# Optimization experiments

Measured on AMD Instinct MI355X. Metric: run time of the kernel, lower is better.

Reference implementation:

```python
import jax, jax.numpy as jnp
import numpy as np

# Architecture constants (from module defaults)
D, H, DH, P, G, DEPTH, M, NCLS = 192, 3, 64, 16, 14, 12, 128, 1000  # M = feature_map_dim // 2
EXITS = (4, 8, 12)
TEMP = 1.0 / np.sqrt(DH)  # Favor softmax_temp = 1/sqrt(d_head)
EPS_ATTN = 1e-6           # fast_transformers LinearAttention eps
LN_EPS = 1e-5


def ln(x, g, b):
    mu = x.mean(-1, keepdims=True)
    var = ((x - mu) ** 2).mean(-1, keepdims=True)
    return (x - mu) * jax.lax.rsqrt(var + LN_EPS) * g + b


def favor(x, omega):
    # FAVOR+ positive random features for the softmax kernel.
    # x: [B,L,H,DH], omega: [DH,M] -> phi: [B,L,H,2M]
    xs = x * np.float32(np.sqrt(TEMP))
    off = 0.5 * (xs * xs).sum(-1, keepdims=True)
    u = jnp.einsum('blhd,dm->blhm', xs, omega)
    phi = jnp.concatenate([jnp.exp(u - off), jnp.exp(-u - off)], axis=-1)
    return phi * np.float32(1.0 / np.sqrt(2 * M))


def forward(x, patch_w, patch_b, pe_ln_g, pe_ln_b, cls_token, pos_embed,
            Wq, bq, Wk, bk, Wv, bv, Wo, bo,
            ln1_g, ln1_b, ln2_g, ln2_b, lnb_g, lnb_b,
            W1, b1, W2, b2, omega, head_w, head_b):
    B = x.shape[0]
    # Patch embedding: Conv2d(k=16, s=16) == blocked einsum
    xp = x.reshape(B, 3, G, P, G, P)
    tok = jnp.einsum('bchpwq,dcpq->bhwd', xp, patch_w).reshape(B, G * G, D) + patch_b
    tok = ln(tok, pe_ln_g, pe_ln_b)  # PatchEmbed.norm (norm_layer=LayerNorm)
    tok = jnp.concatenate([jnp.broadcast_to(cls_token, (B, 1, D)), tok], axis=1) + pos_embed
    xc = tok  # [B, 197, D]
    outs = []
    for i in range(DEPTH):
        # --- linear (FAVOR) attention ---
        q = (xc @ Wq[i].T + bq[i]).reshape(B, -1, H, DH)
        k = (xc @ Wk[i].T + bk[i]).reshape(B, -1, H, DH)
        v = (xc @ Wv[i].T + bv[i]).reshape(B, -1, H, DH)
        Qp = favor(q, omega[i])
        Kp = favor(k, omega[i])
        KV = jnp.einsum('bshm,bshd->bhmd', Kp, v)
        Z = 1.0 / (jnp.einsum('blhm,bhm->blh', Qp, Kp.sum(axis=1)) + EPS_ATTN)
        attn = jnp.einsum('blhm,bhmd,blh->blhd', Qp, KV, Z).reshape(B, -1, D)
        # fast_transformers TransformerEncoderLayer (post-norm style)
        xc = xc + attn @ Wo[i].T + bo[i]
        y = xc = ln(xc, ln1_g[i], ln1_b[i])
        y = jax.nn.relu(y @ W1[i].T + b1[i]) @ W2[i].T + b2[i]
        xc = ln(xc + y, ln2_g[i], ln2_b[i])
        # per-block TransformerEncoder final norm (builder final_normalization)
        xc = ln(xc, lnb_g[i], lnb_b[i])
        if (i + 1) in EXITS:
            j = EXITS.index(i + 1)
            z = xc.mean(axis=1)  # AdaptiveAvgPool1d(1) over sequence
            outs.append(z @ head_w[j].T + head_b[j])
    return tuple(outs)


def setup_inputs() -> dict:
    key = jax.random.key(0)
    ks = iter(jax.random.split(key, 32))
    n = lambda shape, s=0.02: jax.random.normal(next(ks), shape, jnp.float32) * s
    return dict(
        x=jax.random.normal(next(ks), (64, 3, 224, 224), jnp.float32),
        patch_w=n((D, 3, P, P)), patch_b=jnp.zeros((D,), jnp.float32),
        pe_ln_g=jnp.ones((D,), jnp.float32), pe_ln_b=jnp.zeros((D,), jnp.float32),
        cls_token=n((1, 1, D)), pos_embed=n((1, G * G + 1, D)),
        Wq=n((DEPTH, D, D)), bq=jnp.zeros((DEPTH, D), jnp.float32),
        Wk=n((DEPTH, D, D)), bk=jnp.zeros((DEPTH, D), jnp.float32),
        Wv=n((DEPTH, D, D)), bv=jnp.zeros((DEPTH, D), jnp.float32),
        Wo=n((DEPTH, D, D)), bo=jnp.zeros((DEPTH, D), jnp.float32),
        ln1_g=jnp.ones((DEPTH, D), jnp.float32), ln1_b=jnp.zeros((DEPTH, D), jnp.float32),
        ln2_g=jnp.ones((DEPTH, D), jnp.float32), ln2_b=jnp.zeros((DEPTH, D), jnp.float32),
        lnb_g=jnp.ones((DEPTH, D), jnp.float32), lnb_b=jnp.zeros((DEPTH, D), jnp.float32),
        W1=n((DEPTH, 4 * D, D)), b1=jnp.zeros((DEPTH, 4 * D), jnp.float32),
        W2=n((DEPTH, D, 4 * D)), b2=jnp.zeros((DEPTH, D), jnp.float32),
        omega=jax.random.normal(next(ks), (DEPTH, DH, M), jnp.float32),
        head_w=n((len(EXITS), NCLS, D)), head_b=jnp.zeros((len(EXITS), NCLS), jnp.float32),
    )


def reference(x, patch_w, patch_b, pe_ln_g, pe_ln_b, cls_token, pos_embed,
              Wq, bq, Wk, bk, Wv, bv, Wo, bo,
              ln1_g, ln1_b, ln2_g, ln2_b, lnb_g, lnb_b,
              W1, b1, W2, b2, omega, head_w, head_b):
    return forward(x, patch_w, patch_b, pe_ln_g, pe_ln_b, cls_token, pos_embed,
                   Wq, bq, Wk, bk, Wv, bv, Wo, bo,
                   ln1_g, ln1_b, ln2_g, ln2_b, lnb_g, lnb_b,
                   W1, b1, W2, b2, omega, head_w, head_b)
```

## Files before the change

kernel.cpp:

```cpp
#include <hip/hip_runtime.h>
#include <math.h>

#define BB     64
#define LLEN   197
#define BLROWS 12608
#define MPAD   12672
#define DMODEL 192
#define NHEAD  3
#define DHEAD  64
#define M2FEAT 256
#define FFDIM  768
#define NDEPTH 12
#define NCLS   1000
#define NPATCH 196
#define BPROWS 12544
#define KPATCH 768
#define PHIRS  264

#define MODE_PLAIN 0
#define MODE_RELU  1

typedef unsigned short ushort;
typedef __attribute__((ext_vector_type(8))) short bf16x8;
typedef __attribute__((ext_vector_type(4))) float floatx4;
typedef __attribute__((ext_vector_type(4))) short short4v;

__device__ __forceinline__ float wave_reduce_sum(float v) {
#pragma unroll
  for (int s = 32; s > 0; s >>= 1) v += __shfl_xor(v, s, 64);
  return v;
}
__device__ __forceinline__ ushort f2bf(float f) {
  unsigned u = __float_as_uint(f);
  return (ushort)((u + 0x7fffu + ((u >> 16) & 1u)) >> 16);
}
__device__ __forceinline__ float bf2f(ushort u) {
  return __uint_as_float(((unsigned)u) << 16);
}
__device__ __forceinline__ void gll16(const ushort* g, ushort* l) {
  __builtin_amdgcn_global_load_lds(
      (const __attribute__((address_space(1))) void*)g,
      (__attribute__((address_space(3))) void*)l, 16, 0, 0);
}

__global__ __launch_bounds__(256) void gemm_128(
    const ushort* __restrict__ A, int lda,
    const ushort* __restrict__ W, int ldw,
    const float* __restrict__ bias,
    ushort* __restrict__ C, int ldc, int Ndim, int Kdim, int mode)
{
  __shared__ __align__(16) ushort As[2][128 * 32];
  __shared__ __align__(16) ushort Ws[2][128 * 32];
  const int tid = threadIdx.x;
  const int bm = blockIdx.x, bn = blockIdx.y;
  const int wave = tid >> 6, lane = tid & 63;
  const int wm = (wave >> 1) * 64, wn = (wave & 1) * 64;
  const int quad = lane >> 4, l16 = lane & 15;
  const int lrow = lane >> 2, lk = (lane & 3) * 8;
  const ushort* Ap = A + (size_t)(bm * 128) * lda;
  const ushort* Wp = W + (size_t)(bn * 128) * ldw;
  floatx4 acc[4][4] = {};
  const int nT = Kdim >> 5;
#pragma unroll
  for (int t = 0; t < 2; ++t) {
    const int rb = (t * 4 + wave) * 16;
    gll16(Ap + (size_t)(rb + lrow) * lda + lk, &As[0][rb * 32]);
    gll16(Wp + (size_t)(rb + lrow) * ldw + lk, &Ws[0][rb * 32]);
  }
  for (int kt = 0; kt < nT; ++kt) {
    const int cur = kt & 1;
    __syncthreads();
    if (kt + 1 < nT) {
      const int kk = (kt + 1) * 32, nxt = cur ^ 1;
#pragma unroll
      for (int t = 0; t < 2; ++t) {
        const int rb = (t * 4 + wave) * 16;
        gll16(Ap + (size_t)(rb + lrow) * lda + kk + lk, &As[nxt][rb * 32]);
        gll16(Wp + (size_t)(rb + lrow) * ldw + kk + lk, &Ws[nxt][rb * 32]);
      }
    }
    bf16x8 af[4], bf[4];
#pragma unroll
    for (int i = 0; i < 4; ++i) {
      af[i] = *(const bf16x8*)&As[cur][(wm + i * 16 + l16) * 32 + quad * 8];
      bf[i] = *(const bf16x8*)&Ws[cur][(wn + i * 16 + l16) * 32 + quad * 8];
    }
#pragma unroll
    for (int i = 0; i < 4; ++i)
#pragma unroll
      for (int j = 0; j < 4; ++j)
        acc[i][j] = __builtin_amdgcn_mfma_f32_16x16x32_bf16(af[i], bf[j], acc[i][j], 0, 0, 0);
  }
#pragma unroll
  for (int j = 0; j < 4; ++j) {
    const int col = bn * 128 + wn + j * 16 + l16;
    if (col >= Ndim) continue;
    const float bv = bias[col];
#pragma unroll
    for (int i = 0; i < 4; ++i)
#pragma unroll
      for (int r = 0; r < 4; ++r) {
        const int grow = bm * 128 + wm + i * 16 + quad * 4 + r;
        float o = acc[i][j][r] + bv;
        if (mode == MODE_RELU) o = fmaxf(o, 0.f);
        C[(size_t)grow * ldc + col] = f2bf(o);
      }
  }
}

__global__ __launch_bounds__(256) void gemm_bf2(
    const ushort* __restrict__ A, int lda,
    const ushort* __restrict__ W, int ldw,
    const float* __restrict__ bias,
    ushort* __restrict__ C, int ldc, int Kdim, int mode)
{
  __shared__ __align__(16) ushort As[2][128 * 32];
  __shared__ __align__(16) ushort Ws[2][64 * 32];
  const int tid = threadIdx.x;
  const int bm = blockIdx.x, bn = blockIdx.y;
  const int wave = tid >> 6, lane = tid & 63;
  const int wm = (wave >> 1) * 64, wn = (wave & 1) * 32;
  const int quad = lane >> 4, l16 = lane & 15;
  const int lrow = lane >> 2, lk = (lane & 3) * 8;
  const ushort* Ap = A + (size_t)(bm * 128) * lda;
  const ushort* Wp = W + (size_t)(bn * 64) * ldw;
  floatx4 acc[4][2] = {};
  const int nT = Kdim >> 5;
#pragma unroll
  for (int t = 0; t < 2; ++t) {
    const int rb = (t * 4 + wave) * 16;
    gll16(Ap + (size_t)(rb + lrow) * lda + lk, &As[0][rb * 32]);
  }
  gll16(Wp + (size_t)(wave * 16 + lrow) * ldw + lk, &Ws[0][wave * 16 * 32]);
  for (int kt = 0; kt < nT; ++kt) {
    const int cur = kt & 1;
    __syncthreads();
    if (kt + 1 < nT) {
      const int kk = (kt + 1) * 32, nxt = cur ^ 1;
#pragma unroll
      for (int t = 0; t < 2; ++t) {
        const int rb = (t * 4 + wave) * 16;
        gll16(Ap + (size_t)(rb + lrow) * lda + kk + lk, &As[nxt][rb * 32]);
      }
      gll16(Wp + (size_t)(wave * 16 + lrow) * ldw + kk + lk, &Ws[nxt][wave * 16 * 32]);
    }
    bf16x8 af[4], bf[2];
#pragma unroll
    for (int i = 0; i < 4; ++i)
      af[i] = *(const bf16x8*)&As[cur][(wm + i * 16 + l16) * 32 + quad * 8];
#pragma unroll
    for (int j = 0; j < 2; ++j)
      bf[j] = *(const bf16x8*)&Ws[cur][(wn + j * 16 + l16) * 32 + quad * 8];
#pragma unroll
    for (int i = 0; i < 4; ++i)
#pragma unroll
      for (int j = 0; j < 2; ++j)
        acc[i][j] = __builtin_amdgcn_mfma_f32_16x16x32_bf16(af[i], bf[j], acc[i][j], 0, 0, 0);
  }
#pragma unroll
  for (int j = 0; j < 2; ++j) {
    const int col = bn * 64 + wn + j * 16 + l16;
    const float bv = bias[col];
#pragma unroll
    for (int i = 0; i < 4; ++i)
#pragma unroll
      for (int r = 0; r < 4; ++r) {
        const int grow = bm * 128 + wm + i * 16 + quad * 4 + r;
        float o = acc[i][j][r] + bv;
        if (mode == MODE_RELU) o = fmaxf(o, 0.f);
        C[(size_t)grow * ldc + col] = f2bf(o);
      }
  }
}

__global__ __launch_bounds__(256) void gemm_ln(
    const ushort* __restrict__ A, int lda,
    const ushort* __restrict__ W, int ldw,
    const float* __restrict__ bias,
    ushort* __restrict__ XC,
    const float* __restrict__ ga, const float* __restrict__ ba,
    const float* __restrict__ gb, const float* __restrict__ bb,
    int Kdim, int dln)
{
  __shared__ __align__(16) ushort As[2][64 * 32];
  __shared__ __align__(16) ushort Ws[2][192 * 32];
  const int tid = threadIdx.x;
  const int bm = blockIdx.x;
  const int wave = tid >> 6, lane = tid & 63;
  const int quad = lane >> 4, l16 = lane & 15;
  const int lrow = lane >> 2, lk = (lane & 3) * 8;
  const ushort* Ap = A + (size_t)(bm * 64) * lda;
  floatx4 acc[12] = {};
  const int nT = Kdim >> 5;
  gll16(Ap + (size_t)(wave * 16 + lrow) * lda + lk, &As[0][wave * 16 * 32]);
#pragma unroll
  for (int t = 0; t < 3; ++t) {
    const int rb = wave * 48 + t * 16;
    gll16(W + (size_t)(rb + lrow) * ldw + lk, &Ws[0][rb * 32]);
  }
  for (int kt = 0; kt < nT; ++kt) {
    const int cur = kt & 1;
    __syncthreads();
    if (kt + 1 < nT) {
      const int kk = (kt + 1) * 32, nxt = cur ^ 1;
      gll16(Ap + (size_t)(wave * 16 + lrow) * lda + kk + lk, &As[nxt][wave * 16 * 32]);
#pragma unroll
      for (int t = 0; t < 3; ++t) {
        const int rb = wave * 48 + t * 16;
        gll16(W + (size_t)(rb + lrow) * ldw + kk + lk, &Ws[nxt][rb * 32]);
      }
    }
    const bf16x8 af = *(const bf16x8*)&As[cur][(wave * 16 + l16) * 32 + quad * 8];
#pragma unroll
    for (int j = 0; j < 12; ++j) {
      const bf16x8 bf = *(const bf16x8*)&Ws[cur][(j * 16 + l16) * 32 + quad * 8];
      acc[j] = __builtin_amdgcn_mfma_f32_16x16x32_bf16(af, bf, acc[j], 0, 0, 0);
    }
  }
#pragma unroll
  for (int r = 0; r < 4; ++r) {
    const int row = bm * 64 + wave * 16 + quad * 4 + r;
    ushort* xp = XC + (size_t)row * DMODEL;
    float xr[12];
    float s = 0.f, sq = 0.f;
#pragma unroll
    for (int j = 0; j < 12; ++j) {
      const int col = j * 16 + l16;
      const float o = acc[j][r] + bias[col] + bf2f(xp[col]);
      xr[j] = o; s += o; sq += o * o;
    }
#pragma unroll
    for (int m = 1; m < 16; m <<= 1) {
      s += __shfl_xor(s, m, 64); sq += __shfl_xor(sq, m, 64);
    }
    float mu = s * (1.f / 192.f);
    float var = sq * (1.f / 192.f) - mu * mu;
    float rs = rsqrtf(var + 1e-5f);
#pragma unroll
    for (int j = 0; j < 12; ++j) {
      const int col = j * 16 + l16;
      xr[j] = (xr[j] - mu) * rs * ga[col] + ba[col];
    }
    if (dln) {
      float s2 = 0.f, sq2 = 0.f;
#pragma unroll
      for (int j = 0; j < 12; ++j) { s2 += xr[j]; sq2 += xr[j] * xr[j]; }
#pragma unroll
      for (int m = 1; m < 16; m <<= 1) {
        s2 += __shfl_xor(s2, m, 64); sq2 += __shfl_xor(sq2, m, 64);
      }
      mu = s2 * (1.f / 192.f);
      var = sq2 * (1.f / 192.f) - mu * mu;
      rs = rsqrtf(var + 1e-5f);
#pragma unroll
      for (int j = 0; j < 12; ++j) {
        const int col = j * 16 + l16;
        xr[j] = (xr[j] - mu) * rs * gb[col] + bb[col];
      }
    }
#pragma unroll
    for (int j = 0; j < 12; ++j) xp[j * 16 + l16] = f2bf(xr[j]);
  }
}

__global__ __launch_bounds__(256) void kv_fused(
    const ushort* __restrict__ qkv, const ushort* __restrict__ OmT,
    ushort* __restrict__ KVt)
{
  __shared__ __align__(16) ushort Ks[32 * 64];
  __shared__ __align__(16) ushort Vs[32 * 64];
  __shared__ __align__(16) ushort Om[64 * 64];
  __shared__ __align__(16) ushort PhT[128 * 32];
  __shared__ __align__(16) ushort Vts[80 * 32];
  __shared__ float offs[32];
  const int tid = threadIdx.x;
  const int bh = blockIdx.x, mh = blockIdx.y;
  const int b = bh / 3, h = bh - b * 3;
  const int wave = tid >> 6, lane = tid & 63;
  const int quad = lane >> 4, l16 = lane & 15;
  const int lr8 = lane >> 3, lk8 = (lane & 7) * 8;
#pragma unroll
  for (int t = 0; t < 2; ++t) {
    const int rb = (t * 4 + wave) * 8;
    gll16(OmT + (size_t)(mh * 64 + rb + lr8) * 64 + lk8, &Om[rb * 64]);
  }
  {
    const int rb = wave * 8;
    const int l = rb + lr8;
    gll16(qkv + (size_t)(b * 197 + l) * 576 + 192 + h * 64 + lk8, &Ks[rb * 64]);
    gll16(qkv + (size_t)(b * 197 + l) * 576 + 384 + h * 64 + lk8, &Vs[rb * 64]);
  }
  floatx4 acc[2][5] = {};
  for (int c = 0; c < 7; ++c) {
    const int l0 = c * 32;
    __syncthreads();
    if (tid < 64) {
      const int row = tid >> 1, half = tid & 1;
      float s = 0.f;
#pragma unroll
      for (int t = 0; t < 4; ++t) {
        bf16x8 v8 = *(const bf16x8*)&Ks[row * 64 + half * 32 + t * 8];
#pragma unroll
        for (int q = 0; q < 8; ++q) { float xv = bf2f((ushort)v8[q]); s += xv * xv; }
      }
      s += __shfl_xor(s, 1, 64);
      if (half == 0) offs[row] = 0.0625f * s;
    }
    for (int e = tid; e < 80 * 32; e += 256) {
      const int d = e >> 5, ll = e & 31;
      ushort v = 0;
      if (l0 + ll < 197) {
        if (d < 64) v = Vs[ll * 64 + d];
        else if (d == 64) v = 0x3F80;
      }
      Vts[d * 32 + ll] = v;
    }
    floatx4 ui[2] = {};
#pragma unroll
    for (int ks = 0; ks < 64; ks += 32) {
      bf16x8 af[2], bfm;
#pragma unroll
      for (int i = 0; i < 2; ++i)
        af[i] = *(const bf16x8*)&Ks[(i * 16 + l16) * 64 + ks + quad * 8];
      bfm = *(const bf16x8*)&Om[(wave * 16 + l16) * 64 + ks + quad * 8];
#pragma unroll
      for (int i = 0; i < 2; ++i)
        ui[i] = __builtin_amdgcn_mfma_f32_16x16x32_bf16(af[i], bfm, ui[i], 0, 0, 0);
    }
    __syncthreads();
    {
      const int mloc = wave * 16 + l16;
#pragma unroll
      for (int i = 0; i < 2; ++i) {
#pragma unroll
        for (int r = 0; r < 4; ++r) {
          const int ll = i * 16 + quad * 4 + r;
          float ep = 0.f, em = 0.f;
          if (l0 + ll < 197) {
            const float off = offs[ll];
            const float u = ui[i][r];
            ep = __expf(u - off) * 0.0625f;
            em = __expf(-u - off) * 0.0625f;
          }
          PhT[mloc * 32 + ll] = f2bf(ep);
          PhT[(64 + mloc) * 32 + ll] = f2bf(em);
        }
      }
    }
    if (c + 1 < 7) {
      const int rb = wave * 8;
      const int l = (c + 1) * 32 + rb + lr8;
      gll16(qkv + (size_t)(b * 197 + l) * 576 + 192 + h * 64 + lk8, &Ks[rb * 64]);
      gll16(qkv + (size_t)(b * 197 + l) * 576 + 384 + h * 64 + lk8, &Vs[rb * 64]);
    }
    __syncthreads();
    bf16x8 af[2], bf[5];
#pragma unroll
    for (int i = 0; i < 2; ++i)
      af[i] = *(const bf16x8*)&PhT[(wave * 32 + i * 16 + l16) * 32 + quad * 8];
#pragma unroll
    for (int j = 0; j < 5; ++j)
      bf[j] = *(const bf16x8*)&Vts[(j * 16 + l16) * 32 + quad * 8];
#pragma unroll
    for (int i = 0; i < 2; ++i)
#pragma unroll
      for (int j = 0; j < 5; ++j)
        acc[i][j] = __builtin_amdgcn_mfma_f32_16x16x32_bf16(af[i], bf[j], acc[i][j], 0, 0, 0);
  }
#pragma unroll
  for (int i = 0; i < 2; ++i) {
    const int prow0 = wave * 32 + i * 16 + quad * 4;
    const int f0 = (prow0 < 64) ? (mh * 64 + prow0) : (128 + mh * 64 + prow0 - 64);
#pragma unroll
    for (int j = 0; j < 5; ++j) {
      const int d = j * 16 + l16;
      short4v pk;
#pragma unroll
      for (int r = 0; r < 4; ++r) pk[r] = (short)f2bf(acc[i][j][r]);
      *(short4v*)(KVt + ((size_t)bh * 80 + d) * 256 + f0) = pk;
    }
  }
}

__global__ __launch_bounds__(256) void attn_fused(
    const ushort* __restrict__ qkv, const ushort* __restrict__ OmT,
    const ushort* __restrict__ KVt, ushort* __restrict__ OUT)
{
  __shared__ __align__(16) ushort Phi[128 * PHIRS];
  __shared__ __align__(16) ushort Bs[2][80 * 32];
  __shared__ float offs[128];
  __shared__ float zs[128];
  ushort* Qs = Phi;
  ushort* Om = Phi + 128 * 64;
  const int tid = threadIdx.x;
  const int bx = blockIdx.x, bh = blockIdx.y;
  const int b = bh / 3, h = bh - b * 3;
  const int wave = tid >> 6, lane = tid & 63;
  const int wm = (wave >> 1) * 64, wn = (wave & 1) * 64;
  const int quad = lane >> 4, l16 = lane & 15;
  const int lr8 = lane >> 3, lk8 = (lane & 7) * 8;
  const int lrow = lane >> 2, lk = (lane & 3) * 8;
#pragma unroll
  for (int t = 0; t < 4; ++t) {
    const int rb = (t * 4 + wave) * 8;
    const int l = bx * 128 + rb + lr8;
    gll16(qkv + (size_t)(b * 197 + l) * 576 + h * 64 + lk8, &Qs[rb * 64]);
    gll16(OmT + (size_t)(rb + lr8) * 64 + lk8, &Om[rb * 64]);
  }
  __syncthreads();
  {
    const int row = tid >> 1, half = tid & 1;
    float s = 0.f;
#pragma unroll
    for (int t = 0; t < 4; ++t) {
      bf16x8 v8 = *(const bf16x8*)&Qs[row * 64 + half * 32 + t * 8];
#pragma unroll
      for (int q = 0; q < 8; ++q) { float xv = bf2f((ushort)v8[q]); s += xv * xv; }
    }
    s += __shfl_xor(s, 1, 64);
    if (half == 0) offs[row] = 0.0625f * s;
  }
  floatx4 uacc[4][4] = {};
#pragma unroll
  for (int ks = 0; ks < 64; ks += 32) {
    bf16x8 af[4], bf[4];
#pragma unroll
    for (int i = 0; i < 4; ++i) {
      af[i] = *(const bf16x8*)&Qs[(wm + i * 16 + l16) * 64 + ks + quad * 8];
      bf[i] = *(const bf16x8*)&Om[(wn + i * 16 + l16) * 64 + ks + quad * 8];
    }
#pragma unroll
    for (int i = 0; i < 4; ++i)
#pragma unroll
      for (int j = 0; j < 4; ++j)
        uacc[i][j] = __builtin_amdgcn_mfma_f32_16x16x32_bf16(af[i], bf[j], uacc[i][j], 0, 0, 0);
  }
  __syncthreads();
#pragma unroll
  for (int i = 0; i < 4; ++i) {
#pragma unroll
    for (int r = 0; r < 4; ++r) {
      const int l = wm + i * 16 + quad * 4 + r;
      const float off = offs[l];
#pragma unroll
      for (int j = 0; j < 4; ++j) {
        const int m = wn + j * 16 + l16;
        const float u = uacc[i][j][r];
        Phi[l * PHIRS + m]       = f2bf(__expf(u - off)  * 0.0625f);
        Phi[l * PHIRS + m + 128] = f2bf(__expf(-u - off) * 0.0625f);
      }
    }
  }
  const ushort* Bp = KVt + (size_t)bh * 80 * 256;
  gll16(Bp + (size_t)(wave * 16 + lrow) * 256 + lk, &Bs[0][wave * 16 * 32]);
  if (wave == 0) gll16(Bp + (size_t)(64 + lrow) * 256 + lk, &Bs[0][64 * 32]);
  floatx4 acc[2][5] = {};
  for (int c = 0; c < 8; ++c) {
    const int cur = c & 1;
    __syncthreads();
    if (c + 1 < 8) {
      const int m0 = (c + 1) * 32, nxt = cur ^ 1;
      gll16(Bp + (size_t)(wave * 16 + lrow) * 256 + m0 + lk, &Bs[nxt][wave * 16 * 32]);
      if (wave == 0) gll16(Bp + (size_t)(64 + lrow) * 256 + m0 + lk, &Bs[nxt][64 * 32]);
    }
    const int m0 = c * 32;
    bf16x8 af[2], bf[5];
#pragma unroll
    for (int i = 0; i < 2; ++i)
      af[i] = *(const bf16x8*)&Phi[(wave * 32 + i * 16 + l16) * PHIRS + m0 + quad * 8];
#pragma unroll
    for (int j = 0; j < 5; ++j)
      bf[j] = *(const bf16x8*)&Bs[cur][(j * 16 + l16) * 32 + quad * 8];
#pragma unroll
    for (int i = 0; i < 2; ++i)
#pragma unroll
      for (int j = 0; j < 5; ++j)
        acc[i][j] = __builtin_amdgcn_mfma_f32_16x16x32_bf16(af[i], bf[j], acc[i][j], 0, 0, 0);
  }
  if (l16 == 0) {
#pragma unroll
    for (int i = 0; i < 2; ++i)
#pragma unroll
      for (int r = 0; r < 4; ++r)
        zs[wave * 32 + i * 16 + quad * 4 + r] = acc[i][4][r];
  }
  __syncthreads();
#pragma unroll
  for (int i = 0; i < 2; ++i) {
#pragma unroll
    for (int r = 0; r < 4; ++r) {
      const int ll = wave * 32 + i * 16 + quad * 4 + r;
      const int l = bx * 128 + ll;
      if (l >= 197) continue;
      const float z = 1.f / (zs[ll] + 1e-6f);
#pragma unroll
      for (int j = 0; j < 4; ++j)
        OUT[(size_t)(b * 197 + l) * 192 + h * 64 + j * 16 + l16] =
            f2bf(acc[i][j][r] * z);
    }
  }
}

__global__ void conv_qkv(const float* __restrict__ Wq, const float* __restrict__ Wk,
                         const float* __restrict__ Wv, const float* __restrict__ bq,
                         const float* __restrict__ bk, const float* __restrict__ bv,
                         ushort* __restrict__ dst, float* __restrict__ bdst) {
  const int l = blockIdx.y;
  const int e = blockIdx.x * 256 + threadIdx.x;
  const int n = e / 192, k = e - n * 192;
  const float* src;
  if (n < 192)      src = Wq + (size_t)l * 36864 + n * 192;
  else if (n < 384) src = Wk + (size_t)l * 36864 + (n - 192) * 192;
  else              src = Wv + (size_t)l * 36864 + (n - 384) * 192;
  dst[(size_t)l * 640 * 192 + e] = f2bf(src[k]);
  if (e < 576) {
    float bvv;
    if (e < 192)      bvv = bq[l * 192 + e];
    else if (e < 384) bvv = bk[l * 192 + e - 192];
    else              bvv = bv[l * 192 + e - 384];
    bdst[l * 576 + e] = bvv;
  }
}

__global__ void conv_pad(const float* __restrict__ src, ushort* __restrict__ dst,
                         int NK, int padNK) {
  const int l = blockIdx.y;
  const int e = blockIdx.x * 256 + threadIdx.x;
  if (e < NK) dst[(size_t)l * padNK + e] = f2bf(src[(size_t)l * NK + e]);
}

__global__ void conv_omt(const float* __restrict__ om, ushort* __restrict__ dst) {
  const int l = blockIdx.y;
  const int e = blockIdx.x * 256 + threadIdx.x;
  const int m = e >> 6, d = e & 63;
  dst[(size_t)l * 8192 + e] = f2bf(0.35355339059327379f * om[(size_t)l * 8192 + d * 128 + m]);
}

__global__ __launch_bounds__(256) void im2col_kernel(
    const float* __restrict__ X, ushort* __restrict__ Apd)
{
  const int bp = blockIdx.x;
  const int b = bp / NPATCH, p = bp - b * NPATCH;
  const int gh = p / 14, gw = p - gh * 14;
  for (int e = threadIdx.x; e < KPATCH; e += 256) {
    const int c = e >> 8, rem = e & 255, ph = rem >> 4, pw = rem & 15;
    Apd[(size_t)bp * KPATCH + e] =
        f2bf(X[((size_t)(b * 3 + c) * 224 + gh * 16 + ph) * 224 + gw * 16 + pw]);
  }
}

__global__ __launch_bounds__(256) void assemble_kernel(
    const ushort* __restrict__ TK, const float* __restrict__ g,
    const float* __restrict__ bt, const float* __restrict__ cls,
    const float* __restrict__ pos, ushort* __restrict__ XC)
{
  const int w = threadIdx.x >> 6, lane = threadIdx.x & 63;
  const int row = blockIdx.x * 4 + w;
  const int b = row / LLEN, l = row - b * LLEN;
  float o0, o1, o2;
  if (l == 0) {
    o0 = cls[lane]; o1 = cls[lane + 64]; o2 = cls[lane + 128];
  } else {
    const ushort* tp = TK + (size_t)(b * NPATCH + l - 1) * DMODEL;
    const float x0 = bf2f(tp[lane]), x1 = bf2f(tp[lane + 64]), x2 = bf2f(tp[lane + 128]);
    const float s  = wave_reduce_sum(x0 + x1 + x2);
    const float sq = wave_reduce_sum(x0 * x0 + x1 * x1 + x2 * x2);
    const float mu = s * (1.f / 192.f);
    const float var = sq * (1.f / 192.f) - mu * mu;
    const float rs = rsqrtf(var + 1e-5f);
    o0 = (x0 - mu) * rs * g[lane]       + bt[lane];
    o1 = (x1 - mu) * rs * g[lane + 64]  + bt[lane + 64];
    o2 = (x2 - mu) * rs * g[lane + 128] + bt[lane + 128];
  }
  o0 += pos[l * DMODEL + lane];
  o1 += pos[l * DMODEL + lane + 64];
  o2 += pos[l * DMODEL + lane + 128];
  ushort* xp = XC + (size_t)row * DMODEL;
  xp[lane] = f2bf(o0); xp[lane + 64] = f2bf(o1); xp[lane + 128] = f2bf(o2);
}

__global__ __launch_bounds__(192) void pool_kernel(
    const ushort* __restrict__ XC, float* __restrict__ Zp)
{
  const int b = blockIdx.x, d = threadIdx.x;
  float s = 0.f;
#pragma unroll 4
  for (int l = 0; l < LLEN; ++l) s += bf2f(XC[(size_t)(b * LLEN + l) * DMODEL + d]);
  Zp[b * DMODEL + d] = s * (1.f / 197.f);
}

__global__ __launch_bounds__(256) void head_kernel(
    const float* __restrict__ Zp, const float* __restrict__ HW,
    const float* __restrict__ HB, float* __restrict__ OUTp)
{
  const int n = blockIdx.x * 256 + threadIdx.x;
  const int b = blockIdx.y;
  if (n < NCLS) {
    const float* z = Zp + b * DMODEL;
    const float* w = HW + (size_t)n * DMODEL;
    float s = HB[n];
#pragma unroll 4
    for (int d = 0; d < DMODEL; ++d) s = fmaf(z[d], w[d], s);
    OUTp[(size_t)b * NCLS + n] = s;
  }
}

extern "C" void kernel_launch(void* const* d_in, const int* in_sizes, int n_in,
                              void* d_out, int out_size, void* d_ws, size_t ws_size,
                              hipStream_t stream) {
  const float* x        = (const float*)d_in[0];
  const float* patch_w  = (const float*)d_in[1];
  const float* patch_b  = (const float*)d_in[2];
  const float* pe_ln_g  = (const float*)d_in[3];
  const float* pe_ln_b  = (const float*)d_in[4];
  const float* cls_tok  = (const float*)d_in[5];
  const float* pos_emb  = (const float*)d_in[6];
  const float* Wq = (const float*)d_in[7];
  const float* bq = (const float*)d_in[8];
  const float* Wk = (const float*)d_in[9];
  const float* bk = (const float*)d_in[10];
  const float* Wv = (const float*)d_in[11];
  const float* bv = (const float*)d_in[12];
  const float* Wo = (const float*)d_in[13];
  const float* bo = (const float*)d_in[14];
  const float* ln1_g = (const float*)d_in[15];
  const float* ln1_b = (const float*)d_in[16];
  const float* ln2_g = (const float*)d_in[17];
  const float* ln2_b = (const float*)d_in[18];
  const float* lnb_g = (const float*)d_in[19];
  const float* lnb_b = (const float*)d_in[20];
  const float* W1 = (const float*)d_in[21];
  const float* b1 = (const float*)d_in[22];
  const float* W2 = (const float*)d_in[23];
  const float* b2 = (const float*)d_in[24];
  const float* omega  = (const float*)d_in[25];
  const float* head_w = (const float*)d_in[26];
  const float* head_b = (const float*)d_in[27];
  float* out = (float*)d_out;
  char* wsb = (char*)d_ws;

  size_t off = 0;
  auto carve = [&](size_t bytes) { size_t o = off; off += (bytes + 255) & ~(size_t)255; return o; };
  ushort* xc     = (ushort*)(wsb + carve((size_t)MPAD * 192 * 2));
  ushort* qkv    = (ushort*)(wsb + carve((size_t)MPAD * 576 * 2));
  ushort* ab     = (ushort*)(wsb + carve((size_t)MPAD * 192 * 2));
  ushort* hidden = (ushort*)(wsb + carve((size_t)MPAD * 768 * 2));
  ushort* KVt    = (ushort*)(wsb + carve((size_t)192 * 80 * 256 * 2));
  float*  ZPb    = (float*)(wsb + carve((size_t)64 * 192 * 4));
  float*  bqkv   = (float*)(wsb + carve((size_t)12 * 576 * 4));
  ushort* Wqkv_bf = (ushort*)(wsb + carve((size_t)12 * 640 * 192 * 2));
  ushort* Wo_bf   = (ushort*)(wsb + carve((size_t)12 * 256 * 192 * 2));
  ushort* W1_bf   = (ushort*)(wsb + carve((size_t)12 * 768 * 192 * 2));
  ushort* W2_bf   = (ushort*)(wsb + carve((size_t)12 * 256 * 768 * 2));
  ushort* Wp_bf   = (ushort*)(wsb + carve((size_t)256 * 768 * 2));
  ushort* Om_bf   = (ushort*)(wsb + carve((size_t)12 * 128 * 64 * 2));
  ushort* i2c     = hidden;

  conv_qkv<<<dim3(432, 12), 256, 0, stream>>>(Wq, Wk, Wv, bq, bk, bv, Wqkv_bf, bqkv);
  conv_pad<<<dim3(144, 12), 256, 0, stream>>>(Wo, Wo_bf, 36864, 256 * 192);
  conv_pad<<<dim3(576, 12), 256, 0, stream>>>(W1, W1_bf, 147456, 768 * 192);
  conv_pad<<<dim3(576, 12), 256, 0, stream>>>(W2, W2_bf, 147456, 256 * 768);
  conv_pad<<<dim3(576, 1), 256, 0, stream>>>(patch_w, Wp_bf, 147456, 256 * 768);
  conv_omt<<<dim3(32, 12), 256, 0, stream>>>(omega, Om_bf);

  im2col_kernel<<<BPROWS, 256, 0, stream>>>(x, i2c);
  gemm_bf2<<<dim3(98, 3), 256, 0, stream>>>(i2c, KPATCH, Wp_bf, KPATCH,
      patch_b, ab, DMODEL, KPATCH, MODE_PLAIN);
  assemble_kernel<<<BLROWS / 4, 256, 0, stream>>>(ab, pe_ln_g, pe_ln_b,
                                                  cls_tok, pos_emb, xc);

  const int exits[3] = {3, 7, 11};
  for (int i = 0; i < NDEPTH; ++i) {
    gemm_128<<<dim3(99, 5), 256, 0, stream>>>(xc, DMODEL,
        Wqkv_bf + (size_t)i * 640 * 192, DMODEL, bqkv + i * 576,
        qkv, 576, 576, DMODEL, MODE_PLAIN);
    kv_fused<<<dim3(192, 2), 256, 0, stream>>>(qkv,
        Om_bf + (size_t)i * 8192, KVt);
    attn_fused<<<dim3(2, 192), 256, 0, stream>>>(qkv,
        Om_bf + (size_t)i * 8192, KVt, ab);
    gemm_ln<<<MPAD / 64, 256, 0, stream>>>(ab, DMODEL,
        Wo_bf + (size_t)i * 256 * 192, DMODEL, bo + i * DMODEL, xc,
        ln1_g + i * DMODEL, ln1_b + i * DMODEL, nullptr, nullptr,
        DMODEL, 0);
    gemm_128<<<dim3(99, 6), 256, 0, stream>>>(xc, DMODEL,
        W1_bf + (size_t)i * 768 * 192, DMODEL, b1 + i * FFDIM,
        hidden, FFDIM, FFDIM, DMODEL, MODE_RELU);
    gemm_ln<<<MPAD / 64, 256, 0, stream>>>(hidden, FFDIM,
        W2_bf + (size_t)i * 256 * 768, FFDIM, b2 + i * DMODEL, xc,
        ln2_g + i * DMODEL, ln2_b + i * DMODEL,
        lnb_g + i * DMODEL, lnb_b + i * DMODEL,
        FFDIM, 1);
    ln2_fusedless:;

    for (int j = 0; j < 3; ++j) {
      if (i == exits[j]) {
        pool_kernel<<<BB, 192, 0, stream>>>(xc, ZPb);
        head_kernel<<<dim3(4, BB), 256, 0, stream>>>(
            ZPb, head_w + (size_t)j * NCLS * DMODEL, head_b + (size_t)j * NCLS,
            out + (size_t)j * BB * NCLS);
      }
    }
  }
}
```

Before: 1.614 ms.

## Write V transposed from QKV GEMM, swizzle LDS, shrink attn tiles

The QKV GEMM epilogue now writes V directly into a per-(batch,head) transposed buffer, so kv_fused no longer transposes V through shared memory each chunk and can double-buffer V loads. LDS tiles in kv_fused and attn_fused use XOR swizzling and a padded PhT stride to reduce bank conflicts. attn_fused is retiled to 64 rows per block, doubling the grid to improve occupancy. The costs are scattered uncoalesced V stores in the GEMM epilogue, a one-time zeroing kernel for the padded buffer, and more attn blocks that each reload omega.

```diff
diff --git a/kernel.cpp b/kernel.cpp
--- a/kernel.cpp
+++ b/kernel.cpp
@@ -16,9 +16,12 @@
 #define BPROWS 12544
 #define KPATCH 768
 #define PHIRS  264
+#define PHTRS  40
+#define VLT    208
 
 #define MODE_PLAIN 0
 #define MODE_RELU  1
+#define MODE_QKV   2
 
 typedef unsigned short ushort;
 typedef __attribute__((ext_vector_type(8))) short bf16x8;
@@ -43,11 +46,17 @@
       (__attribute__((address_space(3))) void*)l, 16, 0, 0);
 }
 
+__global__ void zero_buf(uint4* __restrict__ p, int n16) {
+  const int i = blockIdx.x * 256 + threadIdx.x;
+  if (i < n16) p[i] = uint4{0, 0, 0, 0};
+}
+
 __global__ __launch_bounds__(256) void gemm_128(
     const ushort* __restrict__ A, int lda,
     const ushort* __restrict__ W, int ldw,
     const float* __restrict__ bias,
-    ushort* __restrict__ C, int ldc, int Ndim, int Kdim, int mode)
+    ushort* __restrict__ C, int ldc, ushort* __restrict__ Vt,
+    int Ndim, int Kdim, int mode)
 {
   __shared__ __align__(16) ushort As[2][128 * 32];
   __shared__ __align__(16) ushort Ws[2][128 * 32];
@@ -91,20 +100,43 @@
       for (int j = 0; j < 4; ++j)
         acc[i][j] = __builtin_amdgcn_mfma_f32_16x16x32_bf16(af[i], bf[j], acc[i][j], 0, 0, 0);
   }
-#pragma unroll
-  for (int j = 0; j < 4; ++j) {
-    const int col = bn * 128 + wn + j * 16 + l16;
-    if (col >= Ndim) continue;
-    const float bv = bias[col];
+  if (mode == MODE_QKV) {
 #pragma unroll
     for (int i = 0; i < 4; ++i)
 #pragma unroll
       for (int r = 0; r < 4; ++r) {
         const int grow = bm * 128 + wm + i * 16 + quad * 4 + r;
-        float o = acc[i][j][r] + bv;
-        if (mode == MODE_RELU) o = fmaxf(o, 0.f);
-        C[(size_t)grow * ldc + col] = f2bf(o);
-      }
+        const int bidx = grow / 197;
+        const int lloc = grow - bidx * 197;
+#pragma unroll
+        for (int j = 0; j < 4; ++j) {
+          const int col = bn * 128 + wn + j * 16 + l16;
+          if (col >= Ndim) continue;
+          const float o = acc[i][j][r] + bias[col];
+          if (col < 384) {
+            C[(size_t)grow * ldc + col] = f2bf(o);
+          } else if (grow < BLROWS) {
+            const int h = (col - 384) >> 6, d = (col - 384) & 63;
+            Vt[((size_t)(bidx * 3 + h) * 64 + d) * VLT + lloc] = f2bf(o);
+          }
+        }
+      }
+  } else {
+#pragma unroll
+    for (int j = 0; j < 4; ++j) {
+      const int col = bn * 128 + wn + j * 16 + l16;
+      if (col >= Ndim) continue;
+      const float bv = bias[col];
+#pragma unroll
+      for (int i = 0; i < 4; ++i)
+#pragma unroll
+        for (int r = 0; r < 4; ++r) {
+          const int grow = bm * 128 + wm + i * 16 + quad * 4 + r;
+          float o = acc[i][j][r] + bv;
+          if (mode == MODE_RELU) o = fmaxf(o, 0.f);
+          C[(size_t)grow * ldc + col] = f2bf(o);
+        }
+    }
   }
 }
 
@@ -265,64 +297,66 @@
 
 __global__ __launch_bounds__(256) void kv_fused(
     const ushort* __restrict__ qkv, const ushort* __restrict__ OmT,
-    ushort* __restrict__ KVt)
+    const ushort* __restrict__ Vt, ushort* __restrict__ KVt)
 {
   __shared__ __align__(16) ushort Ks[32 * 64];
-  __shared__ __align__(16) ushort Vs[32 * 64];
   __shared__ __align__(16) ushort Om[64 * 64];
-  __shared__ __align__(16) ushort PhT[128 * 32];
-  __shared__ __align__(16) ushort Vts[80 * 32];
+  __shared__ __align__(16) ushort PhT[128 * PHTRS];
+  __shared__ __align__(16) ushort Vts[2][64 * 32];
+  __shared__ __align__(16) ushort Vcst[16 * 32];
   __shared__ float offs[32];
   const int tid = threadIdx.x;
   const int bh = blockIdx.x, mh = blockIdx.y;
   const int b = bh / 3, h = bh - b * 3;
   const int wave = tid >> 6, lane = tid & 63;
   const int quad = lane >> 4, l16 = lane & 15;
-  const int lr8 = lane >> 3, lk8 = (lane & 7) * 8;
+  const int lr8 = lane >> 3, g8 = lane & 7;
+  const int lr4 = lane >> 2, g4 = lane & 3;
 #pragma unroll
   for (int t = 0; t < 2; ++t) {
     const int rb = (t * 4 + wave) * 8;
-    gll16(OmT + (size_t)(mh * 64 + rb + lr8) * 64 + lk8, &Om[rb * 64]);
+    const int row = rb + lr8;
+    gll16(OmT + (size_t)(mh * 64 + row) * 64 + ((g8 ^ (row & 7)) * 8), &Om[rb * 64]);
   }
   {
-    const int rb = wave * 8;
-    const int l = rb + lr8;
-    gll16(qkv + (size_t)(b * 197 + l) * 576 + 192 + h * 64 + lk8, &Ks[rb * 64]);
-    gll16(qkv + (size_t)(b * 197 + l) * 576 + 384 + h * 64 + lk8, &Vs[rb * 64]);
-  }
+    const int rowK = wave * 8 + lr8;
+    gll16(qkv + (size_t)(b * 197 + rowK) * 576 + 192 + h * 64 + ((g8 ^ (rowK & 7)) * 8),
+          &Ks[wave * 8 * 64]);
+    const int rowV = wave * 16 + lr4;
+    gll16(Vt + ((size_t)bh * 64 + rowV) * VLT + ((g4 ^ (rowV & 3)) * 8),
+          &Vts[0][wave * 16 * 32]);
+  }
+  for (int e = tid; e < 16 * 32; e += 256) Vcst[e] = (e < 32) ? 0x3F80 : 0;
   floatx4 acc[2][5] = {};
   for (int c = 0; c < 7; ++c) {
     const int l0 = c * 32;
+    const int cur = c & 1;
     __syncthreads();
     if (tid < 64) {
       const int row = tid >> 1, half = tid & 1;
       float s = 0.f;
 #pragma unroll
       for (int t = 0; t < 4; ++t) {
-        bf16x8 v8 = *(const bf16x8*)&Ks[row * 64 + half * 32 + t * 8];
+        bf16x8 v8 = *(const bf16x8*)&Ks[row * 64 + (((half * 4 + t) ^ (row & 7)) * 8)];
 #pragma unroll
         for (int q = 0; q < 8; ++q) { float xv = bf2f((ushort)v8[q]); s += xv * xv; }
       }
       s += __shfl_xor(s, 1, 64);
       if (half == 0) offs[row] = 0.0625f * s;
     }
-    for (int e = tid; e < 80 * 32; e += 256) {
-      const int d = e >> 5, ll = e & 31;
-      ushort v = 0;
-      if (l0 + ll < 197) {
-        if (d < 64) v = Vs[ll * 64 + d];
-        else if (d == 64) v = 0x3F80;
-      }
-      Vts[d * 32 + ll] = v;
-    }
     floatx4 ui[2] = {};
 #pragma unroll
-    for (int ks = 0; ks < 64; ks += 32) {
+    for (int ksb = 0; ksb < 2; ++ksb) {
       bf16x8 af[2], bfm;
 #pragma unroll
-      for (int i = 0; i < 2; ++i)
-        af[i] = *(const bf16x8*)&Ks[(i * 16 + l16) * 64 + ks + quad * 8];
-      bfm = *(const bf16x8*)&Om[(wave * 16 + l16) * 64 + ks + quad * 8];
+      for (int i = 0; i < 2; ++i) {
+        const int row = i * 16 + l16;
+        af[i] = *(const bf16x8*)&Ks[row * 64 + (((quad + (ksb << 2)) ^ (row & 7)) * 8)];
+      }
+      {
+        const int row = wave * 16 + l16;
+        bfm = *(const bf16x8*)&Om[row * 64 + (((quad + (ksb << 2)) ^ (row & 7)) * 8)];
+      }
 #pragma unroll
       for (int i = 0; i < 2; ++i)
         ui[i] = __builtin_amdgcn_mfma_f32_16x16x32_bf16(af[i], bfm, ui[i], 0, 0, 0);
@@ -342,25 +376,31 @@
             ep = __expf(u - off) * 0.0625f;
             em = __expf(-u - off) * 0.0625f;
           }
-          PhT[mloc * 32 + ll] = f2bf(ep);
-          PhT[(64 + mloc) * 32 + ll] = f2bf(em);
+          PhT[mloc * PHTRS + ll] = f2bf(ep);
+          PhT[(64 + mloc) * PHTRS + ll] = f2bf(em);
         }
       }
     }
     if (c + 1 < 7) {
-      const int rb = wave * 8;
-      const int l = (c + 1) * 32 + rb + lr8;
-      gll16(qkv + (size_t)(b * 197 + l) * 576 + 192 + h * 64 + lk8, &Ks[rb * 64]);
-      gll16(qkv + (size_t)(b * 197 + l) * 576 + 384 + h * 64 + lk8, &Vs[rb * 64]);
+      const int rowK = wave * 8 + lr8;
+      const int lK = (c + 1) * 32 + rowK;
+      gll16(qkv + (size_t)(b * 197 + lK) * 576 + 192 + h * 64 + ((g8 ^ (rowK & 7)) * 8),
+            &Ks[wave * 8 * 64]);
+      const int rowV = wave * 16 + lr4;
+      gll16(Vt + ((size_t)bh * 64 + rowV) * VLT + (c + 1) * 32 + ((g4 ^ (rowV & 3)) * 8),
+            &Vts[cur ^ 1][wave * 16 * 32]);
     }
     __syncthreads();
     bf16x8 af[2], bf[5];
 #pragma unroll
     for (int i = 0; i < 2; ++i)
-      af[i] = *(const bf16x8*)&PhT[(wave * 32 + i * 16 + l16) * 32 + quad * 8];
-#pragma unroll
-    for (int j = 0; j < 5; ++j)
-      bf[j] = *(const bf16x8*)&Vts[(j * 16 + l16) * 32 + quad * 8];
+      af[i] = *(const bf16x8*)&PhT[(wave * 32 + i * 16 + l16) * PHTRS + quad * 8];
+#pragma unroll
+    for (int j = 0; j < 4; ++j) {
+      const int row = j * 16 + l16;
+      bf[j] = *(const bf16x8*)&Vts[cur][row * 32 + ((quad ^ (row & 3)) * 8)];
+    }
+    bf[4] = *(const bf16x8*)&Vcst[l16 * 32 + quad * 8];
 #pragma unroll
     for (int i = 0; i < 2; ++i)
 #pragma unroll
@@ -386,118 +426,121 @@
     const ushort* __restrict__ qkv, const ushort* __restrict__ OmT,
     const ushort* __restrict__ KVt, ushort* __restrict__ OUT)
 {
-  __shared__ __align__(16) ushort Phi[128 * PHIRS];
+  __shared__ __align__(16) ushort Phi[64 * PHIRS];
   __shared__ __align__(16) ushort Bs[2][80 * 32];
-  __shared__ float offs[128];
-  __shared__ float zs[128];
+  __shared__ float offs[64];
+  __shared__ float zs[64];
   ushort* Qs = Phi;
-  ushort* Om = Phi + 128 * 64;
+  ushort* Om = Phi + 64 * 64;
   const int tid = threadIdx.x;
   const int bx = blockIdx.x, bh = blockIdx.y;
   const int b = bh / 3, h = bh - b * 3;
   const int wave = tid >> 6, lane = tid & 63;
-  const int wm = (wave >> 1) * 64, wn = (wave & 1) * 64;
   const int quad = lane >> 4, l16 = lane & 15;
-  const int lr8 = lane >> 3, lk8 = (lane & 7) * 8;
-  const int lrow = lane >> 2, lk = (lane & 3) * 8;
+  const int lr8 = lane >> 3, g8 = lane & 7;
+  const int lr4 = lane >> 2, g4 = lane & 3;
+#pragma unroll
+  for (int t = 0; t < 2; ++t) {
+    const int rb = wave * 16 + t * 8;
+    const int row = rb + lr8;
+    const int l = bx * 64 + row;
+    gll16(qkv + (size_t)(b * 197 + l) * 576 + h * 64 + ((g8 ^ (row & 7)) * 8), &Qs[rb * 64]);
+  }
 #pragma unroll
   for (int t = 0; t < 4; ++t) {
-    const int rb = (t * 4 + wave) * 8;
-    const int l = bx * 128 + rb + lr8;
-    gll16(qkv + (size_t)(b * 197 + l) * 576 + h * 64 + lk8, &Qs[rb * 64]);
-    gll16(OmT + (size_t)(rb + lr8) * 64 + lk8, &Om[rb * 64]);
+    const int rb = wave * 32 + t * 8;
+    const int row = rb + lr8;
+    gll16(OmT + (size_t)row * 64 + ((g8 ^ (row & 7)) * 8), &Om[rb * 64]);
   }
   __syncthreads();
-  {
+  if (tid < 128) {
     const int row = tid >> 1, half = tid & 1;
     float s = 0.f;
 #pragma unroll
     for (int t = 0; t < 4; ++t) {
-      bf16x8 v8 = *(const bf16x8*)&Qs[row * 64 + half * 32 + t * 8];
+      bf16x8 v8 = *(const bf16x8*)&Qs[row * 64 + (((half * 4 + t) ^ (row & 7)) * 8)];
 #pragma unroll
       for (int q = 0; q < 8; ++q) { float xv = bf2f((ushort)v8[q]); s += xv * xv; }
     }
     s += __shfl_xor(s, 1, 64);
     if (half == 0) offs[row] = 0.0625f * s;
   }
-  floatx4 uacc[4][4] = {};
-#pragma unroll
-  for (int ks = 0; ks < 64; ks += 32) {
-    bf16x8 af[4], bf[4];
-#pragma unroll
-    for (int i = 0; i < 4; ++i) {
-      af[i] = *(const bf16x8*)&Qs[(wm + i * 16 + l16) * 64 + ks + quad * 8];
-      bf[i] = *(const bf16x8*)&Om[(wn + i * 16 + l16) * 64 + ks + quad * 8];
-    }
-#pragma unroll
-    for (int i = 0; i < 4; ++i)
-#pragma unroll
-      for (int j = 0; j < 4; ++j)
-        uacc[i][j] = __builtin_amdgcn_mfma_f32_16x16x32_bf16(af[i], bf[j], uacc[i][j], 0, 0, 0);
+  floatx4 uacc[8] = {};
+#pragma unroll
+  for (int ksb = 0; ksb < 2; ++ksb) {
+    bf16x8 af, bf[8];
+    {
+      const int row = wave * 16 + l16;
+      af = *(const bf16x8*)&Qs[row * 64 + (((quad + (ksb << 2)) ^ (row & 7)) * 8)];
+    }
+#pragma unroll
+    for (int j = 0; j < 8; ++j) {
+      const int row = j * 16 + l16;
+      bf[j] = *(const bf16x8*)&Om[row * 64 + (((quad + (ksb << 2)) ^ (row & 7)) * 8)];
+    }
+#pragma unroll
+    for (int j = 0; j < 8; ++j)
+      uacc[j] = __builtin_amdgcn_mfma_f32_16x16x32_bf16(af, bf[j], uacc[j], 0, 0, 0);
   }
   __syncthreads();
 #pragma unroll
-  for (int i = 0; i < 4; ++i) {
-#pragma unroll
-    for (int r = 0; r < 4; ++r) {
-      const int l = wm + i * 16 + quad * 4 + r;
-      const float off = offs[l];
-#pragma unroll
-      for (int j = 0; j < 4; ++j) {
-        const int m = wn + j * 16 + l16;
-        const float u = uacc[i][j][r];
-        Phi[l * PHIRS + m]       = f2bf(__expf(u - off)  * 0.0625f);
-        Phi[l * PHIRS + m + 128] = f2bf(__expf(-u - off) * 0.0625f);
-      }
+  for (int r = 0; r < 4; ++r) {
+    const int l = wave * 16 + quad * 4 + r;
+    const float off = offs[l];
+#pragma unroll
+    for (int j = 0; j < 8; ++j) {
+      const int m = j * 16 + l16;
+      const float u = uacc[j][r];
+      Phi[l * PHIRS + m]       = f2bf(__expf(u - off)  * 0.0625f);
+      Phi[l * PHIRS + m + 128] = f2bf(__expf(-u - off) * 0.0625f);
     }
   }
   const ushort* Bp = KVt + (size_t)bh * 80 * 256;
-  gll16(Bp + (size_t)(wave * 16 + lrow) * 256 + lk, &Bs[0][wave * 16 * 32]);
-  if (wave == 0) gll16(Bp + (size_t)(64 + lrow) * 256 + lk, &Bs[0][64 * 32]);
-  floatx4 acc[2][5] = {};
+  {
+    const int row = wave * 16 + lr4;
+    gll16(Bp + (size_t)row * 256 + ((g4 ^ (row & 3)) * 8), &Bs[0][wave * 16 * 32]);
+    if (wave == 0)
+      gll16(Bp + (size_t)(64 + lr4) * 256 + ((g4 ^ (lr4 & 3)) * 8), &Bs[0][64 * 32]);
+  }
+  floatx4 acc[5] = {};
   for (int c = 0; c < 8; ++c) {
     const int cur = c & 1;
     __syncthreads();
     if (c + 1 < 8) {
       const int m0 = (c + 1) * 32, nxt = cur ^ 1;
-      gll16(Bp + (size_t)(wave * 16 + lrow) * 256 + m0 + lk, &Bs[nxt][wave * 16 * 32]);
-      if (wave == 0) gll16(Bp + (size_t)(64 + lrow) * 256 + m0 + lk, &Bs[nxt][64 * 32]);
+      const int row = wave * 16 + lr4;
+      gll16(Bp + (size_t)row * 256 + m0 + ((g4 ^ (row & 3)) * 8), &Bs[nxt][wave * 16 * 32]);
+      if (wave == 0)
+        gll16(Bp + (size_t)(64 + lr4) * 256 + m0 + ((g4 ^ (lr4 & 3)) * 8), &Bs[nxt][64 * 32]);
     }
     const int m0 = c * 32;
-    bf16x8 af[2], bf[5];
-#pragma unroll
-    for (int i = 0; i < 2; ++i)
-      af[i] = *(const bf16x8*)&Phi[(wave * 32 + i * 16 + l16) * PHIRS + m0 + quad * 8];
+    bf16x8 af, bf[5];
+    af = *(const bf16x8*)&Phi[(wave * 16 + l16) * PHIRS + m0 + quad * 8];
+#pragma unroll
+    for (int j = 0; j < 5; ++j) {
+      const int row = j * 16 + l16;
+      bf[j] = *(const bf16x8*)&Bs[cur][row * 32 + ((quad ^ (row & 3)) * 8)];
+    }
 #pragma unroll
     for (int j = 0; j < 5; ++j)
-      bf[j] = *(const bf16x8*)&Bs[cur][(j * 16 + l16) * 32 + quad * 8];
-#pragma unroll
-    for (int i = 0; i < 2; ++i)
-#pragma unroll
-      for (int j = 0; j < 5; ++j)
-        acc[i][j] = __builtin_amdgcn_mfma_f32_16x16x32_bf16(af[i], bf[j], acc[i][j], 0, 0, 0);
+      acc[j] = __builtin_amdgcn_mfma_f32_16x16x32_bf16(af, bf[j], acc[j], 0, 0, 0);
   }
   if (l16 == 0) {
 #pragma unroll
-    for (int i = 0; i < 2; ++i)
-#pragma unroll
-      for (int r = 0; r < 4; ++r)
-        zs[wave * 32 + i * 16 + quad * 4 + r] = acc[i][4][r];
+    for (int r = 0; r < 4; ++r)
+      zs[wave * 16 + quad * 4 + r] = acc[4][r];
   }
   __syncthreads();
 #pragma unroll
-  for (int i = 0; i < 2; ++i) {
-#pragma unroll
-    for (int r = 0; r < 4; ++r) {
-      const int ll = wave * 32 + i * 16 + quad * 4 + r;
-      const int l = bx * 128 + ll;
-      if (l >= 197) continue;
-      const float z = 1.f / (zs[ll] + 1e-6f);
-#pragma unroll
-      for (int j = 0; j < 4; ++j)
-        OUT[(size_t)(b * 197 + l) * 192 + h * 64 + j * 16 + l16] =
-            f2bf(acc[i][j][r] * z);
-    }
+  for (int r = 0; r < 4; ++r) {
+    const int ll = wave * 16 + quad * 4 + r;
+    const int l = bx * 64 + ll;
+    if (l >= 197) continue;
+    const float z = 1.f / (zs[ll] + 1e-6f);
+#pragma unroll
+    for (int j = 0; j < 4; ++j)
+      OUT[(size_t)(b * 197 + l) * 192 + h * 64 + j * 16 + l16] =
+          f2bf(acc[j][r] * z);
   }
 }
 
@@ -646,6 +689,7 @@
   ushort* ab     = (ushort*)(wsb + carve((size_t)MPAD * 192 * 2));
   ushort* hidden = (ushort*)(wsb + carve((size_t)MPAD * 768 * 2));
   ushort* KVt    = (ushort*)(wsb + carve((size_t)192 * 80 * 256 * 2));
+  ushort* Vt     = (ushort*)(wsb + carve((size_t)192 * 64 * VLT * 2 + 1024));
   float*  ZPb    = (float*)(wsb + carve((size_t)64 * 192 * 4));
   float*  bqkv   = (float*)(wsb + carve((size_t)12 * 576 * 4));
   ushort* Wqkv_bf = (ushort*)(wsb + carve((size_t)12 * 640 * 192 * 2));
@@ -656,6 +700,11 @@
   ushort* Om_bf   = (ushort*)(wsb + carve((size_t)12 * 128 * 64 * 2));
   ushort* i2c     = hidden;
 
+  {
+    const int n16 = (int)(((size_t)192 * 64 * VLT * 2 + 1024) / 16);
+    zero_buf<<<(n16 + 255) / 256, 256, 0, stream>>>((uint4*)Vt, n16);
+  }
+
   conv_qkv<<<dim3(432, 12), 256, 0, stream>>>(Wq, Wk, Wv, bq, bk, bv, Wqkv_bf, bqkv);
   conv_pad<<<dim3(144, 12), 256, 0, stream>>>(Wo, Wo_bf, 36864, 256 * 192);
   conv_pad<<<dim3(576, 12), 256, 0, stream>>>(W1, W1_bf, 147456, 768 * 192);
@@ -673,10 +722,10 @@
   for (int i = 0; i < NDEPTH; ++i) {
     gemm_128<<<dim3(99, 5), 256, 0, stream>>>(xc, DMODEL,
         Wqkv_bf + (size_t)i * 640 * 192, DMODEL, bqkv + i * 576,
-        qkv, 576, 576, DMODEL, MODE_PLAIN);
+        qkv, 576, Vt, 576, DMODEL, MODE_QKV);
     kv_fused<<<dim3(192, 2), 256, 0, stream>>>(qkv,
-        Om_bf + (size_t)i * 8192, KVt);
-    attn_fused<<<dim3(2, 192), 256, 0, stream>>>(qkv,
+        Om_bf + (size_t)i * 8192, Vt, KVt);
+    attn_fused<<<dim3(4, 192), 256, 0, stream>>>(qkv,
         Om_bf + (size_t)i * 8192, KVt, ab);
     gemm_ln<<<MPAD / 64, 256, 0, stream>>>(ab, DMODEL,
         Wo_bf + (size_t)i * 256 * 192, DMODEL, bo + i * DMODEL, xc,
@@ -684,13 +733,12 @@
         DMODEL, 0);
     gemm_128<<<dim3(99, 6), 256, 0, stream>>>(xc, DMODEL,
         W1_bf + (size_t)i * 768 * 192, DMODEL, b1 + i * FFDIM,
-        hidden, FFDIM, FFDIM, DMODEL, MODE_RELU);
+        hidden, FFDIM, nullptr, FFDIM, DMODEL, MODE_RELU);
     gemm_ln<<<MPAD / 64, 256, 0, stream>>>(hidden, FFDIM,
         W2_bf + (size_t)i * 256 * 768, FFDIM, b2 + i * DMODEL, xc,
         ln2_g + i * DMODEL, ln2_b + i * DMODEL,
         lnb_g + i * DMODEL, lnb_b + i * DMODEL,
         FFDIM, 1);
-    ln2_fusedless:;
 
     for (int j = 0; j < 3; ++j) {
       if (i == exits[j]) {
```

Result: no change. 1.611 ms (-0.2%).
